# Kernel tuning notes

Measured on AMD Instinct MI355X. Metric: run time of the kernel, lower is better.

The kernel has to match this reference:

```python
import jax, jax.numpy as jnp
import numpy as np

N_NODES = 50000
N_EDGES = 800000
IN_FEATS = 128
OUT_FEATS = 16
NUM_HEADS = 8
NEG_SLOPE = 0.2


def setup_inputs() -> dict:
    key = jax.random.key(0)
    k1, k2, k3, k4, k5 = jax.random.split(key, 5)
    feat = jax.random.normal(k1, (N_NODES, IN_FEATS), dtype=jnp.float32)
    src = jax.random.randint(k2, (N_EDGES,), 0, N_NODES, dtype=jnp.int32)
    dst = jax.random.randint(k3, (N_EDGES,), 0, N_NODES, dtype=jnp.int32)
    # fc weight stored as [in, H*Dout] so y = x @ W (equivalent to torch Linear)
    W = jax.random.normal(k4, (IN_FEATS, NUM_HEADS * OUT_FEATS), dtype=jnp.float32) * 0.05
    attn_weights = jax.random.normal(k5, (2 * NUM_HEADS * OUT_FEATS,), dtype=jnp.float32) * 0.1
    bias = jnp.zeros((NUM_HEADS * OUT_FEATS,), dtype=jnp.float32)
    return {"feat": feat, "W": W, "attn_weights": attn_weights, "bias": bias,
            "src": src, "dst": dst}


def reference(feat, W, attn_weights, bias, src, dst):
    H, D = NUM_HEADS, OUT_FEATS
    N = feat.shape[0]
    # Linear projection: [N, H, D]
    h = (feat @ W).reshape(N, H, D)
    a = attn_weights.reshape(2, H, D)
    # per-node attention logits per head
    e_src = jnp.einsum("nhd,hd->nh", h, a[0])  # source side
    e_dst = jnp.einsum("nhd,hd->nh", h, a[1])  # destination side
    # per-edge scores: [E, H]
    e = e_src[src] + e_dst[dst]
    e = jnp.where(e > 0, e, NEG_SLOPE * e)  # LeakyReLU
    # segment softmax over incoming edges of each dst node
    m = jax.ops.segment_max(e, dst, num_segments=N)          # [N, H]
    m = jnp.where(jnp.isfinite(m), m, 0.0)
    ex = jnp.exp(e - m[dst])                                  # [E, H]
    denom = jax.ops.segment_sum(ex, dst, num_segments=N)     # [N, H]
    alpha = ex / jnp.where(denom[dst] > 0, denom[dst], 1.0)  # [E, H]
    # weighted aggregation of source features: [N, H, D]
    out = jax.ops.segment_sum(alpha[:, :, None] * h[src], dst, num_segments=N)
    out = out + bias.reshape(1, H, D)
    return out
```

## Files before the change

### kernel.cpp

```cpp
#include <hip/hip_runtime.h>
#include <hip/hip_bf16.h>

#define H_HEADS 8
#define D_OUT 16
#define C_FEATS 128
#define NEG_SLOPE 0.2f

typedef __attribute__((ext_vector_type(8))) short short8;
typedef __attribute__((ext_vector_type(4))) float f32x4;

__device__ inline unsigned short f2bf(float f) {
    __hip_bfloat16 b = __float2bfloat16(f);
    return *reinterpret_cast<unsigned short*>(&b);
}
__device__ inline float bf2f(unsigned short u) {
    return __uint_as_float((unsigned)u << 16);
}
__device__ inline float bf_lo(unsigned u) { return __uint_as_float(u << 16); }
__device__ inline float bf_hi(unsigned u) { return __uint_as_float(u & 0xffff0000u); }

__global__ __launch_bounds__(256) void k_prep_deg(const float* __restrict__ W,
                                                  unsigned short* __restrict__ Wfh,
                                                  unsigned short* __restrict__ Wfl,
                                                  const int* __restrict__ dst,
                                                  int* __restrict__ deg,
                                                  int* __restrict__ rank, int E) {
    const int b = blockIdx.x, t = threadIdx.x;
    if (b < 8) {
        const int idx = b * 256 + t;
        const int frag = idx >> 6, lane = idx & 63;
        const int kc = frag >> 3, nt = frag & 7;
        const int kb = kc * 32 + ((lane >> 4) << 3);
        const int col = nt * 16 + (lane & 15);
        unsigned short hs[8], ls[8];
#pragma unroll
        for (int i = 0; i < 8; ++i) {
            const float x = W[(size_t)(kb + i) * C_FEATS + col];
            const unsigned short hh = f2bf(x);
            hs[i] = hh;
            ls[i] = f2bf(x - bf2f(hh));
        }
        uint4 uh, ul;
        uh.x = hs[0] | ((unsigned)hs[1] << 16);
        uh.y = hs[2] | ((unsigned)hs[3] << 16);
        uh.z = hs[4] | ((unsigned)hs[5] << 16);
        uh.w = hs[6] | ((unsigned)hs[7] << 16);
        ul.x = ls[0] | ((unsigned)ls[1] << 16);
        ul.y = ls[2] | ((unsigned)ls[3] << 16);
        ul.z = ls[4] | ((unsigned)ls[5] << 16);
        ul.w = ls[6] | ((unsigned)ls[7] << 16);
        *reinterpret_cast<uint4*>(&Wfh[(size_t)idx * 8]) = uh;
        *reinterpret_cast<uint4*>(&Wfl[(size_t)idx * 8]) = ul;
    } else {
        const int e = (b - 8) * 256 + t;
        if (e < E)
            rank[e] = atomicAdd(&deg[dst[e]], 1);
    }
}

__global__ void k_bsum(const int* __restrict__ deg, int* __restrict__ bsum, int N) {
    int i = blockIdx.x * 256 + threadIdx.x;
    int v = (i < N) ? deg[i] : 0;
#pragma unroll
    for (int m = 1; m < 64; m <<= 1) v += __shfl_xor(v, m, 64);
    __shared__ int ws[4];
    if ((threadIdx.x & 63) == 0) ws[threadIdx.x >> 6] = v;
    __syncthreads();
    if (threadIdx.x == 0) bsum[blockIdx.x] = ws[0] + ws[1] + ws[2] + ws[3];
}

__device__ inline int block_scan_incl(int v) {
    int lane = threadIdx.x & 63, w = threadIdx.x >> 6;
    int x = v;
#pragma unroll
    for (int d = 1; d < 64; d <<= 1) {
        int u = __shfl_up(x, d, 64);
        if (lane >= d) x += u;
    }
    __shared__ int wsum[4];
    if (lane == 63) wsum[w] = x;
    __syncthreads();
    int add = 0;
    for (int k = 0; k < w; ++k) add += wsum[k];
    return x + add;
}

__global__ void k_scanb(const int* __restrict__ bsum, int* __restrict__ bpre,
                        int NB, int* __restrict__ offs, int N) {
    int t = threadIdx.x;
    int v = (t < NB) ? bsum[t] : 0;
    int incl = block_scan_incl(v);
    if (t < NB) bpre[t] = incl - v;
    if (t == NB - 1) offs[N] = incl;
}

__global__ void k_scanc(const int* __restrict__ deg, const int* __restrict__ bpre,
                        int* __restrict__ offs, int N) {
    int i = blockIdx.x * 256 + threadIdx.x;
    int v = (i < N) ? deg[i] : 0;
    int incl = block_scan_incl(v);
    int excl = incl - v + bpre[blockIdx.x];
    if (i < N) offs[i] = excl;
}

__global__ __launch_bounds__(512) void k_gemm_scatter(
    const float* __restrict__ feat, const unsigned short* __restrict__ Wfh,
    const unsigned short* __restrict__ Wfl, const float* __restrict__ aw,
    unsigned short* __restrict__ h16, float* __restrict__ es,
    float* __restrict__ ed, const int* __restrict__ src,
    const int* __restrict__ dst, const int* __restrict__ rank,
    const int* __restrict__ offs, int* __restrict__ ssorted,
    int N, int E, int GB) {
    const int t = threadIdx.x;
    if ((int)blockIdx.x >= GB) {
        const int e = (blockIdx.x - GB) * 512 + t;
        if (e < E)
            ssorted[offs[dst[e]] + rank[e]] = src[e];
        return;
    }
    __shared__ uint4 sW[4096];
    {
        const uint4* gh = reinterpret_cast<const uint4*>(Wfh);
        const uint4* gl = reinterpret_cast<const uint4*>(Wfl);
#pragma unroll
        for (int i = 0; i < 4; ++i) {
            const int j = t + i * 512;
            sW[j] = gh[j];
            sW[j + 2048] = gl[j];
        }
    }
    __syncthreads();

    const int bid = blockIdx.x;
    const int w = t >> 6, lane = t & 63;
    const int rbase = bid * 128 + w * 16;
    const int rowA = rbase + (lane & 15);
    const int ko = (lane >> 4) << 3;
    const bool rv = rowA < N;
    const float* fr = feat + (size_t)rowA * C_FEATS;

    f32x4 acc[8];
#pragma unroll
    for (int nt = 0; nt < 8; ++nt)
#pragma unroll
        for (int j = 0; j < 4; ++j) acc[nt][j] = 0.f;

#pragma unroll
    for (int kc = 0; kc < 4; ++kc) {
        float4 x0 = make_float4(0.f, 0.f, 0.f, 0.f), x1 = x0;
        if (rv) {
            x0 = *reinterpret_cast<const float4*>(fr + kc * 32 + ko);
            x1 = *reinterpret_cast<const float4*>(fr + kc * 32 + ko + 4);
        }
        const float xs[8] = {x0.x, x0.y, x0.z, x0.w, x1.x, x1.y, x1.z, x1.w};
        short8 ah, al;
#pragma unroll
        for (int i = 0; i < 8; ++i) {
            const unsigned short hh = f2bf(xs[i]);
            ah[i] = (short)hh;
            al[i] = (short)f2bf(xs[i] - bf2f(hh));
        }
#pragma unroll
        for (int nt = 0; nt < 8; ++nt) {
            const int fi = (kc * 8 + nt) * 64 + lane;
            const short8 bh = *reinterpret_cast<const short8*>(&sW[fi]);
            const short8 bl = *reinterpret_cast<const short8*>(&sW[fi + 2048]);
            acc[nt] = __builtin_amdgcn_mfma_f32_16x16x32_bf16(ah, bh, acc[nt], 0, 0, 0);
            acc[nt] = __builtin_amdgcn_mfma_f32_16x16x32_bf16(al, bh, acc[nt], 0, 0, 0);
            acc[nt] = __builtin_amdgcn_mfma_f32_16x16x32_bf16(ah, bl, acc[nt], 0, 0, 0);
        }
    }
    const int r0 = rbase + ((lane >> 4) << 2);
    const int colc = lane & 15;
#pragma unroll
    for (int nt = 0; nt < 8; ++nt) {
#pragma unroll
        for (int r = 0; r < 4; ++r) {
            const int row = r0 + r;
            if (row < N)
                h16[(size_t)row * C_FEATS + nt * 16 + colc] = f2bf(acc[nt][r]);
        }
    }
#pragma unroll
    for (int nt = 0; nt < 8; ++nt) {
        const float wa = aw[nt * 16 + colc];
        const float wb = aw[C_FEATS + nt * 16 + colc];
#pragma unroll
        for (int r = 0; r < 4; ++r) {
            float pe = acc[nt][r] * wa;
            float pd = acc[nt][r] * wb;
#pragma unroll
            for (int msk = 1; msk <= 8; msk <<= 1) {
                pe += __shfl_xor(pe, msk, 64);
                pd += __shfl_xor(pd, msk, 64);
            }
            const int row = r0 + r;
            if (colc == 0 && row < N) {
                es[(size_t)row * H_HEADS + nt] = pe;
                ed[(size_t)row * H_HEADS + nt] = pd;
            }
        }
    }
}

__global__ __launch_bounds__(256) void k_agg(const unsigned short* __restrict__ h16,
                                             const float* __restrict__ es,
                                             const float* __restrict__ ed,
                                             const int* __restrict__ offs,
                                             const int* __restrict__ ssorted,
                                             const float* __restrict__ bias,
                                             float* __restrict__ out, int N) {
    const int wid = threadIdx.x >> 6, lane = threadIdx.x & 63;
    const int n = blockIdx.x * 4 + wid;
    if (n >= N) return;
    const int beg = offs[n];
    const int deg = offs[n + 1] - beg;

    const int hh = lane >> 3, j0 = lane & 7;
    const float edv = ed[(size_t)n * H_HEADS + hh];

    const int cl = lane & 15, q = lane >> 4;
    const int ah = cl >> 1;
    const int ab = ah << 3;
    float acc[8];
#pragma unroll
    for (int k = 0; k < 8; ++k) acc[k] = 0.f;

    if (deg <= 32) {
        int snc[4];
#pragma unroll
        for (int c = 0; c < 4; ++c) {
            const int j = c * 8 + j0;
            snc[c] = (j < deg) ? ssorted[beg + j] : 0;
        }
        float evc[4];
#pragma unroll
        for (int c = 0; c < 4; ++c) {
            const int j = c * 8 + j0;
            if (j < deg) {
                float tv = es[(size_t)snc[c] * H_HEADS + hh] + edv;
                evc[c] = tv > 0.f ? tv : NEG_SLOPE * tv;
            } else {
                evc[c] = -1e30f;
            }
        }
        float m = fmaxf(fmaxf(evc[0], evc[1]), fmaxf(evc[2], evc[3]));
#pragma unroll
        for (int msk = 1; msk < 8; msk <<= 1)
            m = fmaxf(m, __shfl_xor(m, msk, 64));
        const float t0 = __expf(evc[0] - m), t1 = __expf(evc[1] - m);
        const float t2 = __expf(evc[2] - m), t3 = __expf(evc[3] - m);
        float s = t0 + t1 + t2 + t3;
#pragma unroll
        for (int msk = 1; msk < 8; msk <<= 1)
            s += __shfl_xor(s, msk, 64);
        const float inv = (s > 0.f) ? 1.f / s : 0.f;
        const float alc[4] = {t0 * inv, t1 * inv, t2 * inv, t3 * inv};

        uint4 hv[8];
        float alv[8];
#pragma unroll
        for (int c = 0; c < 4; ++c) {
#pragma unroll
            for (int e4 = 0; e4 < 2; ++e4) {
                const int idx = c * 2 + e4;
                const int base = c * 8 + e4 * 4;
                if (base < deg) {
                    const int s0 = __shfl(snc[c], 4 * e4 + 0, 64);
                    const int s1 = __shfl(snc[c], 4 * e4 + 1, 64);
                    const int s2 = __shfl(snc[c], 4 * e4 + 2, 64);
                    const int s3 = __shfl(snc[c], 4 * e4 + 3, 64);
                    const int snq = (q == 0) ? s0 : (q == 1) ? s1 : (q == 2) ? s2 : s3;
                    alv[idx] = __shfl(alc[c], ab + 4 * e4 + q, 64);
                    hv[idx] = *reinterpret_cast<const uint4*>(
                        &h16[(size_t)snq * C_FEATS + cl * 8]);
                }
            }
        }
#pragma unroll
        for (int c = 0; c < 4; ++c) {
#pragma unroll
            for (int e4 = 0; e4 < 2; ++e4) {
                const int idx = c * 2 + e4;
                const int base = c * 8 + e4 * 4;
                if (base < deg) {
                    const float al = alv[idx];
                    acc[0] = fmaf(al, bf_lo(hv[idx].x), acc[0]);
                    acc[1] = fmaf(al, bf_hi(hv[idx].x), acc[1]);
                    acc[2] = fmaf(al, bf_lo(hv[idx].y), acc[2]);
                    acc[3] = fmaf(al, bf_hi(hv[idx].y), acc[3]);
                    acc[4] = fmaf(al, bf_lo(hv[idx].z), acc[4]);
                    acc[5] = fmaf(al, bf_hi(hv[idx].z), acc[5]);
                    acc[6] = fmaf(al, bf_lo(hv[idx].w), acc[6]);
                    acc[7] = fmaf(al, bf_hi(hv[idx].w), acc[7]);
                }
            }
        }
    } else {
        float m = -1e30f, s = 0.f;
        for (int e = j0; e < deg; e += 8) {
            int sn = ssorted[beg + e];
            float ev = es[(size_t)sn * H_HEADS + hh] + edv;
            ev = ev > 0.f ? ev : NEG_SLOPE * ev;
            if (ev > m) {
                s = s * __expf(m - ev) + 1.f;
                m = ev;
            } else {
                s += __expf(ev - m);
            }
        }
#pragma unroll
        for (int msk = 1; msk < 8; msk <<= 1) {
            float mo = __shfl_xor(m, msk, 64);
            float so = __shfl_xor(s, msk, 64);
            float mn = fmaxf(m, mo);
            s = s * __expf(m - mn) + so * __expf(mo - mn);
            m = mn;
        }
        const float inv = (s > 0.f) ? 1.f / s : 0.f;

        for (int cb = 0; cb < deg; cb += 8) {
            const int j = cb + j0;
            int sn = 0;
            float alpha = 0.f;
            if (j < deg) {
                sn = ssorted[beg + j];
                float tv = es[(size_t)sn * H_HEADS + hh] + edv;
                tv = tv > 0.f ? tv : NEG_SLOPE * tv;
                alpha = __expf(tv - m) * inv;
            }
            int rem = deg - cb; if (rem > 8) rem = 8;
#pragma unroll
            for (int e4 = 0; e4 < 2; ++e4) {
                if (4 * e4 >= rem) break;
                const int s0 = __shfl(sn, 4 * e4 + 0, 64);
                const int s1 = __shfl(sn, 4 * e4 + 1, 64);
                const int s2 = __shfl(sn, 4 * e4 + 2, 64);
                const int s3 = __shfl(sn, 4 * e4 + 3, 64);
                const int snq = (q == 0) ? s0 : (q == 1) ? s1 : (q == 2) ? s2 : s3;
                const float al = __shfl(alpha, ab + 4 * e4 + q, 64);
                const uint4 hv = *reinterpret_cast<const uint4*>(
                    &h16[(size_t)snq * C_FEATS + cl * 8]);
                acc[0] = fmaf(al, bf_lo(hv.x), acc[0]);
                acc[1] = fmaf(al, bf_hi(hv.x), acc[1]);
                acc[2] = fmaf(al, bf_lo(hv.y), acc[2]);
                acc[3] = fmaf(al, bf_hi(hv.y), acc[3]);
                acc[4] = fmaf(al, bf_lo(hv.z), acc[4]);
                acc[5] = fmaf(al, bf_hi(hv.z), acc[5]);
                acc[6] = fmaf(al, bf_lo(hv.w), acc[6]);
                acc[7] = fmaf(al, bf_hi(hv.w), acc[7]);
            }
        }
    }

#pragma unroll
    for (int k = 0; k < 8; ++k) {
        acc[k] += __shfl_xor(acc[k], 16, 64);
        acc[k] += __shfl_xor(acc[k], 32, 64);
    }
    if (q == 0) {
        const float4 b0 = *reinterpret_cast<const float4*>(&bias[cl * 8]);
        const float4 b1 = *reinterpret_cast<const float4*>(&bias[cl * 8 + 4]);
        float4 o0 = make_float4(acc[0] + b0.x, acc[1] + b0.y, acc[2] + b0.z, acc[3] + b0.w);
        float4 o1 = make_float4(acc[4] + b1.x, acc[5] + b1.y, acc[6] + b1.z, acc[7] + b1.w);
        *reinterpret_cast<float4*>(&out[(size_t)n * C_FEATS + cl * 8]) = o0;
        *reinterpret_cast<float4*>(&out[(size_t)n * C_FEATS + cl * 8 + 4]) = o1;
    }
}

extern "C" void kernel_launch(void* const* d_in, const int* in_sizes, int n_in,
                              void* d_out, int out_size, void* d_ws, size_t ws_size,
                              hipStream_t stream) {
    const float* feat = (const float*)d_in[0];
    const float* W    = (const float*)d_in[1];
    const float* aw   = (const float*)d_in[2];
    const float* bias = (const float*)d_in[3];
    const int*   src  = (const int*)d_in[4];
    const int*   dst  = (const int*)d_in[5];
    float* out = (float*)d_out;

    const int N = in_sizes[0] / C_FEATS;
    const int E = in_sizes[4];
    const int NB = (N + 255) / 256;
    const int GB = (N + 127) / 128;
    const int EB = (E + 255) / 256;
    const int EB2 = (E + 511) / 512;

    char* p = (char*)d_ws;
    auto take = [&](size_t bytes) {
        char* q = p;
        p += (bytes + 255) & ~size_t(255);
        return q;
    };
    unsigned short* h16 = (unsigned short*)take((size_t)N * C_FEATS * 2);
    float* es      = (float*)take((size_t)N * H_HEADS * 4);
    float* edt     = (float*)take((size_t)N * H_HEADS * 4);
    int*   deg     = (int*)take((size_t)N * 4);
    int*   offs    = (int*)take((size_t)(N + 1) * 4);
    int*   bsum    = (int*)take((size_t)NB * 4);
    int*   bpre    = (int*)take((size_t)NB * 4);
    int*   ssorted = (int*)take((size_t)E * 4);
    int*   rank    = (int*)take((size_t)E * 4);
    unsigned short* Wfh = (unsigned short*)take((size_t)C_FEATS * C_FEATS * 2);
    unsigned short* Wfl = (unsigned short*)take((size_t)C_FEATS * C_FEATS * 2);
    (void)ws_size;

    hipMemsetAsync(deg, 0, (size_t)N * 4, stream);
    k_prep_deg<<<8 + EB, 256, 0, stream>>>(W, Wfh, Wfl, dst, deg, rank, E);
    k_bsum<<<NB, 256, 0, stream>>>(deg, bsum, N);
    k_scanb<<<1, 256, 0, stream>>>(bsum, bpre, NB, offs, N);
    k_scanc<<<NB, 256, 0, stream>>>(deg, bpre, offs, N);
    k_gemm_scatter<<<GB + EB2, 512, 0, stream>>>(feat, Wfh, Wfl, aw, h16, es, edt,
                                                 src, dst, rank, offs, ssorted,
                                                 N, E, GB);
    k_agg<<<(N + 3) / 4, 256, 0, stream>>>(h16, es, edt, offs, ssorted, bias, out, N);
}
```

Before: 119.9 us.

## Fuse GEMM with degree counting, drop W low-part split, separate scatter kernel

Moves the GEMM into the first kernel so it runs alongside the degree-counting atomics. Each GEMM block converts W to bf16 in shared memory directly, which removes the separate W preparation pass. The low-order W correction term is dropped, cutting MFMAs per tile from three to two, and the edge scatter becomes its own kernel after the scan. The trade-offs are slightly lower GEMM precision, the W conversion repeated in every block, and one extra kernel launch.

```diff
diff --git a/kernel.cpp b/kernel.cpp
--- a/kernel.cpp
+++ b/kernel.cpp
@@ -19,54 +19,109 @@
 __device__ inline float bf_lo(unsigned u) { return __uint_as_float(u << 16); }
 __device__ inline float bf_hi(unsigned u) { return __uint_as_float(u & 0xffff0000u); }
 
-__global__ __launch_bounds__(256) void k_prep_deg(const float* __restrict__ W,
-                                                  unsigned short* __restrict__ Wfh,
-                                                  unsigned short* __restrict__ Wfl,
-                                                  const int* __restrict__ dst,
-                                                  int* __restrict__ deg,
-                                                  int* __restrict__ rank, int E) {
-    const int b = blockIdx.x, t = threadIdx.x;
-    if (b < 8) {
-        const int idx = b * 256 + t;
-        const int frag = idx >> 6, lane = idx & 63;
-        const int kc = frag >> 3, nt = frag & 7;
-        const int kb = kc * 32 + ((lane >> 4) << 3);
-        const int col = nt * 16 + (lane & 15);
-        unsigned short hs[8], ls[8];
+__global__ __launch_bounds__(512) void k_gemm_deg(
+    const float* __restrict__ feat, const float* __restrict__ W,
+    const float* __restrict__ aw, const int* __restrict__ dst,
+    int* __restrict__ deg, int* __restrict__ rank,
+    unsigned short* __restrict__ h16, float* __restrict__ es,
+    float* __restrict__ ed, int N, int E, int DB) {
+    const int t = threadIdx.x;
+    if ((int)blockIdx.x < DB) {
+        const int stride = DB * 512;
+        for (int e = blockIdx.x * 512 + t; e < E; e += stride)
+            rank[e] = atomicAdd(&deg[dst[e]], 1);
+        return;
+    }
+    __shared__ uint4 sW[2048];
+    {
+#pragma unroll
+        for (int i = 0; i < 4; ++i) {
+            const int j = t + i * 512;
+            const int frag = j >> 6, l2 = j & 63;
+            const int kc = frag >> 3, nt = frag & 7;
+            const int kb = kc * 32 + ((l2 >> 4) << 3);
+            const int col = nt * 16 + (l2 & 15);
+            unsigned short hs[8];
+#pragma unroll
+            for (int ii = 0; ii < 8; ++ii)
+                hs[ii] = f2bf(W[(size_t)(kb + ii) * C_FEATS + col]);
+            uint4 uh;
+            uh.x = hs[0] | ((unsigned)hs[1] << 16);
+            uh.y = hs[2] | ((unsigned)hs[3] << 16);
+            uh.z = hs[4] | ((unsigned)hs[5] << 16);
+            uh.w = hs[6] | ((unsigned)hs[7] << 16);
+            sW[j] = uh;
+        }
+    }
+    __syncthreads();
+
+    const int bid = blockIdx.x - DB;
+    const int w = t >> 6, lane = t & 63;
+    const int rbase = bid * 128 + w * 16;
+    const int rowA = rbase + (lane & 15);
+    const int ko = (lane >> 4) << 3;
+    const bool rv = rowA < N;
+    const float* fr = feat + (size_t)rowA * C_FEATS;
+
+    f32x4 acc[8];
+#pragma unroll
+    for (int nt = 0; nt < 8; ++nt)
+#pragma unroll
+        for (int j = 0; j < 4; ++j) acc[nt][j] = 0.f;
+
+#pragma unroll
+    for (int kc = 0; kc < 4; ++kc) {
+        float4 x0 = make_float4(0.f, 0.f, 0.f, 0.f), x1 = x0;
+        if (rv) {
+            x0 = *reinterpret_cast<const float4*>(fr + kc * 32 + ko);
+            x1 = *reinterpret_cast<const float4*>(fr + kc * 32 + ko + 4);
+        }
+        const float xs[8] = {x0.x, x0.y, x0.z, x0.w, x1.x, x1.y, x1.z, x1.w};
+        short8 ah, al;
 #pragma unroll
         for (int i = 0; i < 8; ++i) {
-            const float x = W[(size_t)(kb + i) * C_FEATS + col];
-            const unsigned short hh = f2bf(x);
-            hs[i] = hh;
-            ls[i] = f2bf(x - bf2f(hh));
-        }
-        uint4 uh, ul;
-        uh.x = hs[0] | ((unsigned)hs[1] << 16);
-        uh.y = hs[2] | ((unsigned)hs[3] << 16);
-        uh.z = hs[4] | ((unsigned)hs[5] << 16);
-        uh.w = hs[6] | ((unsigned)hs[7] << 16);
-        ul.x = ls[0] | ((unsigned)ls[1] << 16);
-        ul.y = ls[2] | ((unsigned)ls[3] << 16);
-        ul.z = ls[4] | ((unsigned)ls[5] << 16);
-        ul.w = ls[6] | ((unsigned)ls[7] << 16);
-        *reinterpret_cast<uint4*>(&Wfh[(size_t)idx * 8]) = uh;
-        *reinterpret_cast<uint4*>(&Wfl[(size_t)idx * 8]) = ul;
-    } else {
-        const int e = (b - 8) * 256 + t;
-        if (e < E)
-            rank[e] = atomicAdd(&deg[dst[e]], 1);
-    }
-}
-
-__global__ void k_bsum(const int* __restrict__ deg, int* __restrict__ bsum, int N) {
-    int i = blockIdx.x * 256 + threadIdx.x;
-    int v = (i < N) ? deg[i] : 0;
-#pragma unroll
-    for (int m = 1; m < 64; m <<= 1) v += __shfl_xor(v, m, 64);
-    __shared__ int ws[4];
-    if ((threadIdx.x & 63) == 0) ws[threadIdx.x >> 6] = v;
-    __syncthreads();
-    if (threadIdx.x == 0) bsum[blockIdx.x] = ws[0] + ws[1] + ws[2] + ws[3];
+            const unsigned short hh = f2bf(xs[i]);
+            ah[i] = (short)hh;
+            al[i] = (short)f2bf(xs[i] - bf2f(hh));
+        }
+#pragma unroll
+        for (int nt = 0; nt < 8; ++nt) {
+            const short8 bh = *reinterpret_cast<const short8*>(&sW[(kc * 8 + nt) * 64 + lane]);
+            acc[nt] = __builtin_amdgcn_mfma_f32_16x16x32_bf16(ah, bh, acc[nt], 0, 0, 0);
+            acc[nt] = __builtin_amdgcn_mfma_f32_16x16x32_bf16(al, bh, acc[nt], 0, 0, 0);
+        }
+    }
+    const int r0 = rbase + ((lane >> 4) << 2);
+    const int colc = lane & 15;
+#pragma unroll
+    for (int nt = 0; nt < 8; ++nt) {
+#pragma unroll
+        for (int r = 0; r < 4; ++r) {
+            const int row = r0 + r;
+            if (row < N)
+                h16[(size_t)row * C_FEATS + nt * 16 + colc] = f2bf(acc[nt][r]);
+        }
+    }
+#pragma unroll
+    for (int nt = 0; nt < 8; ++nt) {
+        const float wa = aw[nt * 16 + colc];
+        const float wb = aw[C_FEATS + nt * 16 + colc];
+#pragma unroll
+        for (int r = 0; r < 4; ++r) {
+            float pe = acc[nt][r] * wa;
+            float pd = acc[nt][r] * wb;
+#pragma unroll
+            for (int msk = 1; msk <= 8; msk <<= 1) {
+                pe += __shfl_xor(pe, msk, 64);
+                pd += __shfl_xor(pd, msk, 64);
+            }
+            const int row = r0 + r;
+            if (colc == 0 && row < N) {
+                es[(size_t)row * H_HEADS + nt] = pe;
+                ed[(size_t)row * H_HEADS + nt] = pd;
+            }
+        }
+    }
 }
 
 __device__ inline int block_scan_incl(int v) {
@@ -83,6 +138,17 @@
     int add = 0;
     for (int k = 0; k < w; ++k) add += wsum[k];
     return x + add;
+}
+
+__global__ void k_bsum(const int* __restrict__ deg, int* __restrict__ bsum, int N) {
+    int i = blockIdx.x * 256 + threadIdx.x;
+    int v = (i < N) ? deg[i] : 0;
+#pragma unroll
+    for (int m = 1; m < 64; m <<= 1) v += __shfl_xor(v, m, 64);
+    __shared__ int ws[4];
+    if ((threadIdx.x & 63) == 0) ws[threadIdx.x >> 6] = v;
+    __syncthreads();
+    if (threadIdx.x == 0) bsum[blockIdx.x] = ws[0] + ws[1] + ws[2] + ws[3];
 }
 
 __global__ void k_scanb(const int* __restrict__ bsum, int* __restrict__ bpre,
@@ -103,104 +169,12 @@
     if (i < N) offs[i] = excl;
 }
 
-__global__ __launch_bounds__(512) void k_gemm_scatter(
-    const float* __restrict__ feat, const unsigned short* __restrict__ Wfh,
-    const unsigned short* __restrict__ Wfl, const float* __restrict__ aw,
-    unsigned short* __restrict__ h16, float* __restrict__ es,
-    float* __restrict__ ed, const int* __restrict__ src,
-    const int* __restrict__ dst, const int* __restrict__ rank,
-    const int* __restrict__ offs, int* __restrict__ ssorted,
-    int N, int E, int GB) {
-    const int t = threadIdx.x;
-    if ((int)blockIdx.x >= GB) {
-        const int e = (blockIdx.x - GB) * 512 + t;
-        if (e < E)
-            ssorted[offs[dst[e]] + rank[e]] = src[e];
-        return;
-    }
-    __shared__ uint4 sW[4096];
-    {
-        const uint4* gh = reinterpret_cast<const uint4*>(Wfh);
-        const uint4* gl = reinterpret_cast<const uint4*>(Wfl);
-#pragma unroll
-        for (int i = 0; i < 4; ++i) {
-            const int j = t + i * 512;
-            sW[j] = gh[j];
-            sW[j + 2048] = gl[j];
-        }
-    }
-    __syncthreads();
-
-    const int bid = blockIdx.x;
-    const int w = t >> 6, lane = t & 63;
-    const int rbase = bid * 128 + w * 16;
-    const int rowA = rbase + (lane & 15);
-    const int ko = (lane >> 4) << 3;
-    const bool rv = rowA < N;
-    const float* fr = feat + (size_t)rowA * C_FEATS;
-
-    f32x4 acc[8];
-#pragma unroll
-    for (int nt = 0; nt < 8; ++nt)
-#pragma unroll
-        for (int j = 0; j < 4; ++j) acc[nt][j] = 0.f;
-
-#pragma unroll
-    for (int kc = 0; kc < 4; ++kc) {
-        float4 x0 = make_float4(0.f, 0.f, 0.f, 0.f), x1 = x0;
-        if (rv) {
-            x0 = *reinterpret_cast<const float4*>(fr + kc * 32 + ko);
-            x1 = *reinterpret_cast<const float4*>(fr + kc * 32 + ko + 4);
-        }
-        const float xs[8] = {x0.x, x0.y, x0.z, x0.w, x1.x, x1.y, x1.z, x1.w};
-        short8 ah, al;
-#pragma unroll
-        for (int i = 0; i < 8; ++i) {
-            const unsigned short hh = f2bf(xs[i]);
-            ah[i] = (short)hh;
-            al[i] = (short)f2bf(xs[i] - bf2f(hh));
-        }
-#pragma unroll
-        for (int nt = 0; nt < 8; ++nt) {
-            const int fi = (kc * 8 + nt) * 64 + lane;
-            const short8 bh = *reinterpret_cast<const short8*>(&sW[fi]);
-            const short8 bl = *reinterpret_cast<const short8*>(&sW[fi + 2048]);
-            acc[nt] = __builtin_amdgcn_mfma_f32_16x16x32_bf16(ah, bh, acc[nt], 0, 0, 0);
-            acc[nt] = __builtin_amdgcn_mfma_f32_16x16x32_bf16(al, bh, acc[nt], 0, 0, 0);
-            acc[nt] = __builtin_amdgcn_mfma_f32_16x16x32_bf16(ah, bl, acc[nt], 0, 0, 0);
-        }
-    }
-    const int r0 = rbase + ((lane >> 4) << 2);
-    const int colc = lane & 15;
-#pragma unroll
-    for (int nt = 0; nt < 8; ++nt) {
-#pragma unroll
-        for (int r = 0; r < 4; ++r) {
-            const int row = r0 + r;
-            if (row < N)
-                h16[(size_t)row * C_FEATS + nt * 16 + colc] = f2bf(acc[nt][r]);
-        }
-    }
-#pragma unroll
-    for (int nt = 0; nt < 8; ++nt) {
-        const float wa = aw[nt * 16 + colc];
-        const float wb = aw[C_FEATS + nt * 16 + colc];
-#pragma unroll
-        for (int r = 0; r < 4; ++r) {
-            float pe = acc[nt][r] * wa;
-            float pd = acc[nt][r] * wb;
-#pragma unroll
-            for (int msk = 1; msk <= 8; msk <<= 1) {
-                pe += __shfl_xor(pe, msk, 64);
-                pd += __shfl_xor(pd, msk, 64);
-            }
-            const int row = r0 + r;
-            if (colc == 0 && row < N) {
-                es[(size_t)row * H_HEADS + nt] = pe;
-                ed[(size_t)row * H_HEADS + nt] = pd;
-            }
-        }
-    }
+__global__ void k_scatter(const int* __restrict__ src, const int* __restrict__ dst,
+                          const int* __restrict__ rank, const int* __restrict__ offs,
+                          int* __restrict__ ssorted, int E) {
+    int e = blockIdx.x * 256 + threadIdx.x;
+    if (e < E)
+        ssorted[offs[dst[e]] + rank[e]] = src[e];
 }
 
 __global__ __launch_bounds__(256) void k_agg(const unsigned short* __restrict__ h16,
@@ -383,8 +357,8 @@
     const int E = in_sizes[4];
     const int NB = (N + 255) / 256;
     const int GB = (N + 127) / 128;
+    const int DB = 256;
     const int EB = (E + 255) / 256;
-    const int EB2 = (E + 511) / 512;
 
     char* p = (char*)d_ws;
     auto take = [&](size_t bytes) {
@@ -401,17 +375,14 @@
     int*   bpre    = (int*)take((size_t)NB * 4);
     int*   ssorted = (int*)take((size_t)E * 4);
     int*   rank    = (int*)take((size_t)E * 4);
-    unsigned short* Wfh = (unsigned short*)take((size_t)C_FEATS * C_FEATS * 2);
-    unsigned short* Wfl = (unsigned short*)take((size_t)C_FEATS * C_FEATS * 2);
     (void)ws_size;
 
     hipMemsetAsync(deg, 0, (size_t)N * 4, stream);
-    k_prep_deg<<<8 + EB, 256, 0, stream>>>(W, Wfh, Wfl, dst, deg, rank, E);
+    k_gemm_deg<<<DB + GB, 512, 0, stream>>>(feat, W, aw, dst, deg, rank,
+                                            h16, es, edt, N, E, DB);
     k_bsum<<<NB, 256, 0, stream>>>(deg, bsum, N);
     k_scanb<<<1, 256, 0, stream>>>(bsum, bpre, NB, offs, N);
     k_scanc<<<NB, 256, 0, stream>>>(deg, bpre, offs, N);
-    k_gemm_scatter<<<GB + EB2, 512, 0, stream>>>(feat, Wfh, Wfl, aw, h16, es, edt,
-                                                 src, dst, rank, offs, ssorted,
-                                                 N, E, GB);
+    k_scatter<<<EB, 256, 0, stream>>>(src, dst, rank, offs, ssorted, E);
     k_agg<<<(N + 3) / 4, 256, 0, stream>>>(h16, es, edt, offs, ssorted, bias, out, N);
 }
```

New measurement: 121.9 us. About the same (+1.6%).
